# Kernel tuning notes

Hardware: AMD Instinct MI355X
Metric: run time of the kernel (lower is better)

The kernel has to match this reference:

```python
import jax, jax.numpy as jnp
import numpy as np

TEMP = 1.0
EPS = 1e-6


def trop_linear(x, w, b, temp=TEMP):
    # x: (..., in), w: (out, in) -> (..., out)
    # y_i = temp * logsumexp_j((w_ij + x_j)/temp) + b_i  (soft tropical / max-plus)
    z = x[..., None, :] + w  # (..., out, in)
    y = temp * jax.nn.logsumexp(z / temp, axis=-1)
    return y + b


def trop_layernorm(x, weight, bias, eps=EPS):
    n = x.shape[-1]
    # torch.median returns the lower of the two middle elements for even n
    med = jnp.sort(x, axis=-1)[..., (n - 1) // 2][..., None]
    q75 = jnp.quantile(x, 0.75, axis=-1, keepdims=True)
    q25 = jnp.quantile(x, 0.25, axis=-1, keepdims=True)
    iqr = jnp.maximum(q75 - q25, eps)
    return (x - med) / iqr * weight + bias


def setup_inputs() -> dict:
    key = jax.random.key(0)
    ks = jax.random.split(key, 8)
    B, D_IN, D_H, D_OUT = 1024, 512, 512, 256
    return {
        "x": jax.random.normal(ks[0], (B, D_IN), dtype=jnp.float32),
        "w1": 0.1 * jax.random.normal(ks[1], (D_H, D_IN), dtype=jnp.float32),
        "b1": jnp.zeros((D_H,), dtype=jnp.float32),
        "ln1_w": jnp.ones((D_H,), dtype=jnp.float32),
        "ln1_b": jnp.zeros((D_H,), dtype=jnp.float32),
        "w2": 0.1 * jax.random.normal(ks[2], (D_H, D_H), dtype=jnp.float32),
        "b2": jnp.zeros((D_H,), dtype=jnp.float32),
        "ln2_w": jnp.ones((D_H,), dtype=jnp.float32),
        "ln2_b": jnp.zeros((D_H,), dtype=jnp.float32),
        "w3": 0.1 * jax.random.normal(ks[3], (D_OUT, D_H), dtype=jnp.float32),
        "b3": jnp.zeros((D_OUT,), dtype=jnp.float32),
    }


def reference(x, w1, b1, ln1_w, ln1_b, w2, b2, ln2_w, ln2_b, w3, b3):
    h = trop_linear(x, w1, b1)
    h = trop_layernorm(h, ln1_w, ln1_b)
    h = jnp.maximum(h, 0.0)  # TropicalActivation('relu', threshold=0)
    h = trop_linear(h, w2, b2)
    h = trop_layernorm(h, ln2_w, ln2_b)
    h = jnp.maximum(h, 0.0)
    return trop_linear(h, w3, b3)
```

## Files before the change

### kernel.cpp

```cpp
#include <hip/hip_runtime.h>
#include <math.h>


typedef float v4f __attribute__((ext_vector_type(4)));

#define ELS_B 528
#define LN64f 4.1588830833596715f

__device__ __forceinline__ int pk4_fp8(float a, float b, float c, float d) {
    int p = __builtin_amdgcn_cvt_pk_fp8_f32(a, b, 0, 0);
    p = __builtin_amdgcn_cvt_pk_fp8_f32(c, d, p, 1);
    return p;
}

__global__ __launch_bounds__(256) void expW_frag(const float* __restrict__ w1,
                                                 const float* __restrict__ w2,
                                                 const float* __restrict__ w3,
                                                 uint8_t* __restrict__ Ef) {
    int u = blockIdx.x * 256 + threadIdx.x;
    int lane = u & 63, t = (u >> 6) & 15, S = u >> 10;
    int r = lane & 15, q = lane >> 4;
    const float* w; int tile;
    if (S < 32)      { w = w1; tile = S; }
    else if (S < 64) { w = w2; tile = S - 32; }
    else             { w = w3; tile = S - 64; }
    const float* src = w + (tile * 16 + r) * 512 + t * 32 + q * 8;
    float4 a = *reinterpret_cast<const float4*>(src);
    float4 b = *reinterpret_cast<const float4*>(src + 4);
    int2 o;
    o.x = pk4_fp8(__expf(a.x), __expf(a.y), __expf(a.z), __expf(a.w));
    o.y = pk4_fp8(__expf(b.x), __expf(b.y), __expf(b.z), __expf(b.w));
    *reinterpret_cast<int2*>(Ef + u * 8) = o;
}

__device__ __forceinline__ void load_areg(const uint8_t* Els, int lane, long* areg) {
    const uint8_t* ap = Els + (lane & 1) * ELS_B + ((lane >> 4) & 3) * 8;
#pragma unroll
    for (int t = 0; t < 16; ++t)
        areg[t] = *reinterpret_cast<const long*>(ap + t * 32);
}

template <int NSUB>
__device__ __forceinline__ void prefetchB(const uint8_t* __restrict__ bp,
                                          int s0, long bb[8][4]) {
#pragma unroll
    for (int p = 0; p < 8; ++p)
#pragma unroll
        for (int s = 0; s < NSUB; ++s)
            bb[p][s] = *reinterpret_cast<const long*>(bp + ((s0 + s) * 16 + p) * 512);
}

template <int NSUB>
__device__ __forceinline__ void gemm_body(const uint8_t* __restrict__ bp,
                                          int s0, const long* areg,
                                          long bb[8][4], v4f* acc) {
#pragma unroll
    for (int s = 0; s < NSUB; ++s) acc[s] = (v4f){0.f, 0.f, 0.f, 0.f};
#pragma unroll
    for (int t = 0; t < 16; ++t) {
        long a = areg[t];
        long bcur[NSUB];
#pragma unroll
        for (int s = 0; s < NSUB; ++s) bcur[s] = bb[t & 7][s];
        if (t < 8) {
#pragma unroll
            for (int s = 0; s < NSUB; ++s)
                bb[t & 7][s] =
                    *reinterpret_cast<const long*>(bp + ((s0 + s) * 16 + t + 8) * 512);
        }
#pragma unroll
        for (int s = 0; s < NSUB; ++s)
            acc[s] = __builtin_amdgcn_mfma_f32_16x16x32_fp8_fp8(a, bcur[s],
                                                                acc[s], 0, 0, 0);
    }
}

__device__ __forceinline__ void ln_row(const float* hbuf,
                                       const float* __restrict__ lw,
                                       const float* __restrict__ lb,
                                       uint8_t* Els, float* crow,
                                       int w, int lane) {
    const float4* lw4 = reinterpret_cast<const float4*>(lw + lane * 8);
    const float4* lb4 = reinterpret_cast<const float4*>(lb + lane * 8);
    float4 wa = lw4[0], wb = lw4[1], ba = lb4[0], bbv = lb4[1];

    float h[8], v[8];
    {
        const float* hp = hbuf + w * 512 + lane * 8;
        float4 a = *reinterpret_cast<const float4*>(hp);
        float4 b = *reinterpret_cast<const float4*>(hp + 4);
        h[0] = a.x; h[1] = a.y; h[2] = a.z; h[3] = a.w;
        h[4] = b.x; h[5] = b.y; h[6] = b.z; h[7] = b.w;
#pragma unroll
        for (int j = 0; j < 8; ++j) v[j] = h[j];
    }
#pragma clang loop unroll(disable)
    for (int k = 2; k <= 512; k <<= 1) {
#pragma clang loop unroll(disable)
        for (int jj = (k >> 1); jj > 0; jj >>= 1) {
            if (jj >= 8) {
                int lm = jj >> 3;
                bool low = ((lane & lm) == 0);
#pragma unroll
                for (int j = 0; j < 8; ++j) {
                    float pv = __shfl_xor(v[j], lm);
                    bool up = ((((lane << 3) | j) & k) == 0);
                    v[j] = (up == low) ? fminf(v[j], pv) : fmaxf(v[j], pv);
                }
            } else if (jj == 4) {
#pragma unroll
                for (int j = 0; j < 4; ++j) {
                    bool up = ((((lane << 3) | j) & k) == 0);
                    float a = v[j], c = v[j + 4];
                    float lo = fminf(a, c), hi = fmaxf(a, c);
                    v[j] = up ? lo : hi;
                    v[j + 4] = up ? hi : lo;
                }
            } else if (jj == 2) {
#pragma unroll
                for (int jb = 0; jb < 8; jb += 4)
#pragma unroll
                    for (int j0 = 0; j0 < 2; ++j0) {
                        int j = jb + j0;
                        bool up = ((((lane << 3) | j) & k) == 0);
                        float a = v[j], c = v[j + 2];
                        float lo = fminf(a, c), hi = fmaxf(a, c);
                        v[j] = up ? lo : hi;
                        v[j + 2] = up ? hi : lo;
                    }
            } else {
#pragma unroll
                for (int j = 0; j < 8; j += 2) {
                    bool up = ((((lane << 3) | j) & k) == 0);
                    float a = v[j], c = v[j + 1];
                    float lo = fminf(a, c), hi = fmaxf(a, c);
                    v[j] = up ? lo : hi;
                    v[j + 1] = up ? hi : lo;
                }
            }
        }
    }
    float s127 = __shfl(v[7], 15);
    float s128 = __shfl(v[0], 16);
    float med  = __shfl(v[7], 31);
    float s383 = __shfl(v[7], 47);
    float s384 = __shfl(v[0], 48);
    float q25 = s127 + 0.75f * (s128 - s127);
    float q75 = s383 + 0.25f * (s384 - s383);
    float inv = 1.0f / fmaxf(q75 - q25, 1e-6f);

    float y[8], cm = 0.0f;
    {
        float lwv[8] = {wa.x, wa.y, wa.z, wa.w, wb.x, wb.y, wb.z, wb.w};
        float lbv[8] = {ba.x, ba.y, ba.z, ba.w, bbv.x, bbv.y, bbv.z, bbv.w};
#pragma unroll
        for (int j = 0; j < 8; ++j) {
            y[j] = fmaxf((h[j] - med) * inv * lwv[j] + lbv[j], 0.0f);
            cm = fmaxf(cm, y[j]);
        }
    }
#pragma unroll
    for (int s = 32; s > 0; s >>= 1) cm = fmaxf(cm, __shfl_xor(cm, s));
    {
        float e[8];
#pragma unroll
        for (int j = 0; j < 8; ++j) e[j] = 64.0f * __expf(y[j] - cm);
        int2 o;
        o.x = pk4_fp8(e[0], e[1], e[2], e[3]);
        o.y = pk4_fp8(e[4], e[5], e[6], e[7]);
        *reinterpret_cast<int2*>(&Els[w * ELS_B + lane * 8]) = o;
    }
    if (lane == 0) crow[w] = cm;
}

__global__ __launch_bounds__(512, 4) void fused_rows(
    const float* __restrict__ x,
    const float* __restrict__ b1,
    const float* __restrict__ ln1w, const float* __restrict__ ln1b,
    const float* __restrict__ b2,
    const float* __restrict__ ln2w, const float* __restrict__ ln2b,
    const float* __restrict__ b3,
    const uint8_t* __restrict__ Ew,
    float* __restrict__ out)
{
    __shared__ uint8_t Els[2 * ELS_B];
    __shared__ float hbuf[2 * 512];
    __shared__ float crow[2];

    const int tid = threadIdx.x;
    const int lane = tid & 63;
    const int w = tid >> 6;
    const int r = lane & 15, q = lane >> 4;
    const int blk = blockIdx.x;

    const uint8_t* bp1 = Ew + lane * 8;
    const uint8_t* bp2 = bp1 + 262144;
    const uint8_t* bp3 = bp1 + 524288;

    long bb[8][4];
    long areg[16];
    v4f acc[4];

    prefetchB<4>(bp1, w * 4, bb);

    if (tid < 256) {
        int row = tid >> 7, col = (tid & 127) * 4;
        float4 a = *reinterpret_cast<const float4*>(x + blk * 1024 + row * 512 + col);
        *reinterpret_cast<int*>(&Els[row * ELS_B + col]) =
            pk4_fp8(4.0f * __expf(a.x), 4.0f * __expf(a.y),
                    4.0f * __expf(a.z), 4.0f * __expf(a.w));
    }
    __syncthreads();

    load_areg(Els, lane, areg);
    gemm_body<4>(bp1, w * 4, areg, bb, acc);
    if (q == 0) {
#pragma unroll
        for (int s = 0; s < 4; ++s) {
            int col = (w * 4 + s) * 16 + r;
            float bbv = b1[col];
#pragma unroll
            for (int t = 0; t < 2; ++t)
                hbuf[t * 512 + col] = __logf(acc[s][t]) + bbv;
        }
    }
    prefetchB<4>(bp2, w * 4, bb);
    __syncthreads();
    if (w < 2) ln_row(hbuf, ln1w, ln1b, Els, crow, w, lane);
    __syncthreads();

    load_areg(Els, lane, areg);
    gemm_body<4>(bp2, w * 4, areg, bb, acc);
    if (q == 0) {
#pragma unroll
        for (int s = 0; s < 4; ++s) {
            int col = (w * 4 + s) * 16 + r;
            float bbv = b2[col];
#pragma unroll
            for (int t = 0; t < 2; ++t)
                hbuf[t * 512 + col] = __logf(acc[s][t]) + bbv;
        }
    }
    prefetchB<2>(bp3, w * 2, bb);
    __syncthreads();
    if (w < 2) ln_row(hbuf, ln2w, ln2b, Els, crow, w, lane);
    __syncthreads();

    load_areg(Els, lane, areg);
    gemm_body<2>(bp3, w * 2, areg, bb, acc);
    if (q == 0) {
#pragma unroll
        for (int s = 0; s < 2; ++s) {
            int col = (w * 2 + s) * 16 + r;
            float bbv = b3[col] - LN64f;
#pragma unroll
            for (int t = 0; t < 2; ++t)
                out[(blk * 2 + t) * 256 + col] = __logf(acc[s][t]) + crow[t] + bbv;
        }
    }
}

extern "C" void kernel_launch(void* const* d_in, const int* in_sizes, int n_in,
                              void* d_out, int out_size, void* d_ws, size_t ws_size,
                              hipStream_t stream) {
    const float* x    = (const float*)d_in[0];
    const float* w1   = (const float*)d_in[1];
    const float* b1   = (const float*)d_in[2];
    const float* ln1w = (const float*)d_in[3];
    const float* ln1b = (const float*)d_in[4];
    const float* w2   = (const float*)d_in[5];
    const float* b2   = (const float*)d_in[6];
    const float* ln2w = (const float*)d_in[7];
    const float* ln2b = (const float*)d_in[8];
    const float* w3   = (const float*)d_in[9];
    const float* b3   = (const float*)d_in[10];
    float* out = (float*)d_out;

    uint8_t* Ew = (uint8_t*)d_ws;

    expW_frag<<<320, 256, 0, stream>>>(w1, w2, w3, Ew);
    fused_rows<<<512, 512, 0, stream>>>(x, b1, ln1w, ln1b, b2, ln2w, ln2b,
                                        b3, Ew, out);
}
```

Baseline: 111.8 us.

## Split fused per-row kernel into separate tiled GEMM and layernorm kernels

Replaces the single fused kernel, which handled 2 rows per 512-thread block and wasted most of each 16-row MFMA tile, with a chain of kernels. Each GEMM now fills full 16-row fp8 MFMA tiles, and layernorm runs as its own kernel that writes fragment-layout fp8 activations. The input exp/fp8 conversion moves into the prep kernel. The aim is better MFMA utilization and fewer redundant weight loads per row, at the cost of more launches and global round trips for the intermediates.

```diff
diff --git a/kernel.cpp b/kernel.cpp
--- a/kernel.cpp
+++ b/kernel.cpp
@@ -4,7 +4,6 @@
 
 typedef float v4f __attribute__((ext_vector_type(4)));
 
-#define ELS_B 528
 #define LN64f 4.1588830833596715f
 
 __device__ __forceinline__ int pk4_fp8(float a, float b, float c, float d) {
@@ -13,98 +12,142 @@
     return p;
 }
 
-__global__ __launch_bounds__(256) void expW_frag(const float* __restrict__ w1,
+__global__ __launch_bounds__(256) void prep_frag(const float* __restrict__ w1,
                                                  const float* __restrict__ w2,
                                                  const float* __restrict__ w3,
-                                                 uint8_t* __restrict__ Ef) {
+                                                 const float* __restrict__ x,
+                                                 uint8_t* __restrict__ Ew,
+                                                 uint8_t* __restrict__ Ax) {
     int u = blockIdx.x * 256 + threadIdx.x;
     int lane = u & 63, t = (u >> 6) & 15, S = u >> 10;
     int r = lane & 15, q = lane >> 4;
-    const float* w; int tile;
-    if (S < 32)      { w = w1; tile = S; }
-    else if (S < 64) { w = w2; tile = S - 32; }
-    else             { w = w3; tile = S - 64; }
-    const float* src = w + (tile * 16 + r) * 512 + t * 32 + q * 8;
+    const float* m; int tile; uint8_t* dst; float sc;
+    if (S < 32)      { m = w1; tile = S;      dst = Ew;          sc = 1.0f; }
+    else if (S < 64) { m = w2; tile = S - 32; dst = Ew + 262144; sc = 1.0f; }
+    else if (S < 80) { m = w3; tile = S - 64; dst = Ew + 524288; sc = 1.0f; }
+    else             { m = x;  tile = S - 80; dst = Ax;          sc = 4.0f; }
+    const float* src = m + (tile * 16 + r) * 512 + t * 32 + q * 8;
     float4 a = *reinterpret_cast<const float4*>(src);
     float4 b = *reinterpret_cast<const float4*>(src + 4);
     int2 o;
-    o.x = pk4_fp8(__expf(a.x), __expf(a.y), __expf(a.z), __expf(a.w));
-    o.y = pk4_fp8(__expf(b.x), __expf(b.y), __expf(b.z), __expf(b.w));
-    *reinterpret_cast<int2*>(Ef + u * 8) = o;
-}
-
-__device__ __forceinline__ void load_areg(const uint8_t* Els, int lane, long* areg) {
-    const uint8_t* ap = Els + (lane & 1) * ELS_B + ((lane >> 4) & 3) * 8;
+    o.x = pk4_fp8(sc * __expf(a.x), sc * __expf(a.y),
+                  sc * __expf(a.z), sc * __expf(a.w));
+    o.y = pk4_fp8(sc * __expf(b.x), sc * __expf(b.y),
+                  sc * __expf(b.z), sc * __expf(b.w));
+    *reinterpret_cast<int2*>(dst + (tile * 16 + t) * 512 + lane * 8) = o;
+}
+
+__device__ __forceinline__ void gemm_k512(const uint8_t* __restrict__ ap,
+                                          const uint8_t* __restrict__ bp,
+                                          int s0, v4f* acc) {
+    long areg[16];
+    long bb[8][4];
 #pragma unroll
     for (int t = 0; t < 16; ++t)
-        areg[t] = *reinterpret_cast<const long*>(ap + t * 32);
-}
-
-template <int NSUB>
-__device__ __forceinline__ void prefetchB(const uint8_t* __restrict__ bp,
-                                          int s0, long bb[8][4]) {
+        areg[t] = *reinterpret_cast<const long*>(ap + t * 512);
 #pragma unroll
     for (int p = 0; p < 8; ++p)
 #pragma unroll
-        for (int s = 0; s < NSUB; ++s)
+        for (int s = 0; s < 4; ++s)
             bb[p][s] = *reinterpret_cast<const long*>(bp + ((s0 + s) * 16 + p) * 512);
-}
-
-template <int NSUB>
-__device__ __forceinline__ void gemm_body(const uint8_t* __restrict__ bp,
-                                          int s0, const long* areg,
-                                          long bb[8][4], v4f* acc) {
-#pragma unroll
-    for (int s = 0; s < NSUB; ++s) acc[s] = (v4f){0.f, 0.f, 0.f, 0.f};
+#pragma unroll
+    for (int s = 0; s < 4; ++s) acc[s] = (v4f){0.f, 0.f, 0.f, 0.f};
 #pragma unroll
     for (int t = 0; t < 16; ++t) {
         long a = areg[t];
-        long bcur[NSUB];
-#pragma unroll
-        for (int s = 0; s < NSUB; ++s) bcur[s] = bb[t & 7][s];
+        long bcur[4];
+#pragma unroll
+        for (int s = 0; s < 4; ++s) bcur[s] = bb[t & 7][s];
         if (t < 8) {
 #pragma unroll
-            for (int s = 0; s < NSUB; ++s)
+            for (int s = 0; s < 4; ++s)
                 bb[t & 7][s] =
                     *reinterpret_cast<const long*>(bp + ((s0 + s) * 16 + t + 8) * 512);
         }
 #pragma unroll
-        for (int s = 0; s < NSUB; ++s)
+        for (int s = 0; s < 4; ++s)
             acc[s] = __builtin_amdgcn_mfma_f32_16x16x32_fp8_fp8(a, bcur[s],
                                                                 acc[s], 0, 0, 0);
     }
 }
 
-__device__ __forceinline__ void ln_row(const float* hbuf,
-                                       const float* __restrict__ lw,
-                                       const float* __restrict__ lb,
-                                       uint8_t* Els, float* crow,
-                                       int w, int lane) {
+__global__ __launch_bounds__(64) void gemm_h(const uint8_t* __restrict__ Af,
+                                             const uint8_t* __restrict__ Bf,
+                                             const float* __restrict__ bias,
+                                             float* __restrict__ h) {
+    int Wv = blockIdx.x;
+    int m = Wv >> 3, n64 = Wv & 7;
+    int lane = threadIdx.x;
+    int r = lane & 15, q = lane >> 4;
+    v4f acc[4];
+    gemm_k512(Af + m * 8192 + lane * 8, Bf + lane * 8, n64 * 4, acc);
+#pragma unroll
+    for (int s = 0; s < 4; ++s) {
+        int col = (n64 * 4 + s) * 16 + r;
+        float bv = bias[col];
+#pragma unroll
+        for (int tt = 0; tt < 4; ++tt)
+            h[(m * 16 + q * 4 + tt) * 512 + col] = __logf(acc[s][tt]) + bv;
+    }
+}
+
+__global__ __launch_bounds__(64) void gemm_out(const uint8_t* __restrict__ Af,
+                                               const uint8_t* __restrict__ Bf,
+                                               const float* __restrict__ b3,
+                                               const float* __restrict__ crow,
+                                               float* __restrict__ out) {
+    int Wv = blockIdx.x;
+    int m = Wv >> 2, n64 = Wv & 3;
+    int lane = threadIdx.x;
+    int r = lane & 15, q = lane >> 4;
+    v4f acc[4];
+    gemm_k512(Af + m * 8192 + lane * 8, Bf + lane * 8, n64 * 4, acc);
+#pragma unroll
+    for (int s = 0; s < 4; ++s) {
+        int col = (n64 * 4 + s) * 16 + r;
+        float bv = b3[col] - LN64f;
+#pragma unroll
+        for (int tt = 0; tt < 4; ++tt) {
+            int row = m * 16 + q * 4 + tt;
+            out[row * 256 + col] = __logf(acc[s][tt]) + crow[row] + bv;
+        }
+    }
+}
+
+__global__ __launch_bounds__(256) void ln_rows(const float* __restrict__ h,
+                                               const float* __restrict__ lw,
+                                               const float* __restrict__ lb,
+                                               uint8_t* __restrict__ Aout,
+                                               float* __restrict__ crow) {
+    int w = threadIdx.x >> 6, lane = threadIdx.x & 63;
+    int rho = blockIdx.x * 4 + w;
+
     const float4* lw4 = reinterpret_cast<const float4*>(lw + lane * 8);
     const float4* lb4 = reinterpret_cast<const float4*>(lb + lane * 8);
     float4 wa = lw4[0], wb = lw4[1], ba = lb4[0], bbv = lb4[1];
 
-    float h[8], v[8];
+    float hv[8], v[8];
     {
-        const float* hp = hbuf + w * 512 + lane * 8;
+        const float* hp = h + rho * 512 + lane * 8;
         float4 a = *reinterpret_cast<const float4*>(hp);
         float4 b = *reinterpret_cast<const float4*>(hp + 4);
-        h[0] = a.x; h[1] = a.y; h[2] = a.z; h[3] = a.w;
-        h[4] = b.x; h[5] = b.y; h[6] = b.z; h[7] = b.w;
-#pragma unroll
-        for (int j = 0; j < 8; ++j) v[j] = h[j];
+        hv[0] = a.x; hv[1] = a.y; hv[2] = a.z; hv[3] = a.w;
+        hv[4] = b.x; hv[5] = b.y; hv[6] = b.z; hv[7] = b.w;
+#pragma unroll
+        for (int j = 0; j < 8; ++j) v[j] = hv[j];
     }
 #pragma clang loop unroll(disable)
     for (int k = 2; k <= 512; k <<= 1) {
 #pragma clang loop unroll(disable)
-        for (int jj = (k >> 1); jj > 0; jj >>= 1) {
+        for (int jj = 256; jj > 0; jj >>= 1) {
+            if (jj >= k) continue;
             if (jj >= 8) {
                 int lm = jj >> 3;
-                bool low = ((lane & lm) == 0);
 #pragma unroll
                 for (int j = 0; j < 8; ++j) {
                     float pv = __shfl_xor(v[j], lm);
                     bool up = ((((lane << 3) | j) & k) == 0);
+                    bool low = ((lane & lm) == 0);
                     v[j] = (up == low) ? fminf(v[j], pv) : fmaxf(v[j], pv);
                 }
             } else if (jj == 4) {
@@ -155,7 +198,7 @@
         float lbv[8] = {ba.x, ba.y, ba.z, ba.w, bbv.x, bbv.y, bbv.z, bbv.w};
 #pragma unroll
         for (int j = 0; j < 8; ++j) {
-            y[j] = fmaxf((h[j] - med) * inv * lwv[j] + lbv[j], 0.0f);
+            y[j] = fmaxf((hv[j] - med) * inv * lwv[j] + lbv[j], 0.0f);
             cm = fmaxf(cm, y[j]);
         }
     }
@@ -168,96 +211,11 @@
         int2 o;
         o.x = pk4_fp8(e[0], e[1], e[2], e[3]);
         o.y = pk4_fp8(e[4], e[5], e[6], e[7]);
-        *reinterpret_cast<int2*>(&Els[w * ELS_B + lane * 8]) = o;
-    }
-    if (lane == 0) crow[w] = cm;
-}
-
-__global__ __launch_bounds__(512, 4) void fused_rows(
-    const float* __restrict__ x,
-    const float* __restrict__ b1,
-    const float* __restrict__ ln1w, const float* __restrict__ ln1b,
-    const float* __restrict__ b2,
-    const float* __restrict__ ln2w, const float* __restrict__ ln2b,
-    const float* __restrict__ b3,
-    const uint8_t* __restrict__ Ew,
-    float* __restrict__ out)
-{
-    __shared__ uint8_t Els[2 * ELS_B];
-    __shared__ float hbuf[2 * 512];
-    __shared__ float crow[2];
-
-    const int tid = threadIdx.x;
-    const int lane = tid & 63;
-    const int w = tid >> 6;
-    const int r = lane & 15, q = lane >> 4;
-    const int blk = blockIdx.x;
-
-    const uint8_t* bp1 = Ew + lane * 8;
-    const uint8_t* bp2 = bp1 + 262144;
-    const uint8_t* bp3 = bp1 + 524288;
-
-    long bb[8][4];
-    long areg[16];
-    v4f acc[4];
-
-    prefetchB<4>(bp1, w * 4, bb);
-
-    if (tid < 256) {
-        int row = tid >> 7, col = (tid & 127) * 4;
-        float4 a = *reinterpret_cast<const float4*>(x + blk * 1024 + row * 512 + col);
-        *reinterpret_cast<int*>(&Els[row * ELS_B + col]) =
-            pk4_fp8(4.0f * __expf(a.x), 4.0f * __expf(a.y),
-                    4.0f * __expf(a.z), 4.0f * __expf(a.w));
-    }
-    __syncthreads();
-
-    load_areg(Els, lane, areg);
-    gemm_body<4>(bp1, w * 4, areg, bb, acc);
-    if (q == 0) {
-#pragma unroll
-        for (int s = 0; s < 4; ++s) {
-            int col = (w * 4 + s) * 16 + r;
-            float bbv = b1[col];
-#pragma unroll
-            for (int t = 0; t < 2; ++t)
-                hbuf[t * 512 + col] = __logf(acc[s][t]) + bbv;
-        }
-    }
-    prefetchB<4>(bp2, w * 4, bb);
-    __syncthreads();
-    if (w < 2) ln_row(hbuf, ln1w, ln1b, Els, crow, w, lane);
-    __syncthreads();
-
-    load_areg(Els, lane, areg);
-    gemm_body<4>(bp2, w * 4, areg, bb, acc);
-    if (q == 0) {
-#pragma unroll
-        for (int s = 0; s < 4; ++s) {
-            int col = (w * 4 + s) * 16 + r;
-            float bbv = b2[col];
-#pragma unroll
-            for (int t = 0; t < 2; ++t)
-                hbuf[t * 512 + col] = __logf(acc[s][t]) + bbv;
-        }
-    }
-    prefetchB<2>(bp3, w * 2, bb);
-    __syncthreads();
-    if (w < 2) ln_row(hbuf, ln2w, ln2b, Els, crow, w, lane);
-    __syncthreads();
-
-    load_areg(Els, lane, areg);
-    gemm_body<2>(bp3, w * 2, areg, bb, acc);
-    if (q == 0) {
-#pragma unroll
-        for (int s = 0; s < 2; ++s) {
-            int col = (w * 2 + s) * 16 + r;
-            float bbv = b3[col] - LN64f;
-#pragma unroll
-            for (int t = 0; t < 2; ++t)
-                out[(blk * 2 + t) * 256 + col] = __logf(acc[s][t]) + crow[t] + bbv;
-        }
-    }
+        uint8_t* dst = Aout + ((rho >> 4) * 16 + (lane >> 2)) * 512
+                            + ((lane & 3) * 16 + (rho & 15)) * 8;
+        *reinterpret_cast<int2*>(dst) = o;
+    }
+    if (lane == 0) crow[rho] = cm;
 }
 
 extern "C" void kernel_launch(void* const* d_in, const int* in_sizes, int n_in,
@@ -276,9 +234,18 @@
     const float* b3   = (const float*)d_in[10];
     float* out = (float*)d_out;
 
-    uint8_t* Ew = (uint8_t*)d_ws;
-
-    expW_frag<<<320, 256, 0, stream>>>(w1, w2, w3, Ew);
-    fused_rows<<<512, 512, 0, stream>>>(x, b1, ln1w, ln1b, b2, ln2w, ln2b,
-                                        b3, Ew, out);
-}
+    uint8_t* ws = (uint8_t*)d_ws;
+    uint8_t* Ew   = ws;
+    uint8_t* A1   = ws + (1u << 20);
+    uint8_t* A2   = ws + (1u << 20) + 524288;
+    uint8_t* A3   = ws + (2u << 20);
+    float*   h    = (float*)(ws + (2u << 20) + 524288);
+    float*   crow = (float*)(ws + (5u << 20));
+
+    prep_frag<<<576, 256, 0, stream>>>(w1, w2, w3, x, Ew, A1);
+    gemm_h<<<512, 64, 0, stream>>>(A1, Ew, b1, h);
+    ln_rows<<<256, 256, 0, stream>>>(h, ln1w, ln1b, A2, crow);
+    gemm_h<<<512, 64, 0, stream>>>(A2, Ew + 262144, b2, h);
+    ln_rows<<<256, 256, 0, stream>>>(h, ln2w, ln2b, A3, crow);
+    gemm_out<<<256, 64, 0, stream>>>(A3, Ew + 524288, b3, crow, out);
+}
```

New measurement: 115.3 us. 1.03x slower.
